# Kernel optimization log

Hardware: AMD Instinct MI355X
Metric: run time of the kernel (lower is better)

The kernel has to match this reference:

```python
import jax, jax.numpy as jnp
import numpy as np

CH_IN, CH_Y = 32, 16
B, H, W = 16, 256, 256


def setup_inputs() -> dict:
    key = jax.random.key(0)
    ks = jax.random.split(key, 10)
    scale_in = 1.0 / np.sqrt(CH_IN)
    scale_y = 1.0 / np.sqrt(CH_Y)
    return {
        "c": jax.random.normal(ks[0], (B, CH_IN, H, W), dtype=jnp.float32),
        "p": jax.random.normal(ks[1], (B, CH_IN, H, W), dtype=jnp.float32),
        "Wq": jax.random.uniform(ks[2], (CH_Y, CH_IN), jnp.float32, -scale_in, scale_in),
        "bq": jax.random.uniform(ks[3], (CH_Y,), jnp.float32, -scale_in, scale_in),
        "Wk": jax.random.uniform(ks[4], (CH_Y, CH_IN), jnp.float32, -scale_in, scale_in),
        "bk": jax.random.uniform(ks[5], (CH_Y,), jnp.float32, -scale_in, scale_in),
        "Wv": jax.random.uniform(ks[6], (CH_Y, CH_IN), jnp.float32, -scale_in, scale_in),
        "bv": jax.random.uniform(ks[7], (CH_Y,), jnp.float32, -scale_in, scale_in),
        "Wy": jax.random.uniform(ks[8], (CH_IN, CH_Y), jnp.float32, -scale_y, scale_y),
        "by": jax.random.uniform(ks[9], (CH_IN,), jnp.float32, -scale_y, scale_y),
    }


def _conv1x1(x, w, b):
    # x: [B,C,H,W], w: [O,C], b: [O] -> [B,O,H,W]
    return jnp.einsum("bchw,oc->bohw", x, w) + b[None, :, None, None]


def reference(c, p, Wq, bq, Wk, bk, Wv, bv, Wy, by):
    q = _conv1x1(c, Wq, bq)
    k = _conv1x1(p, Wk, bk)
    v = _conv1x1(p, Wv, bv)
    y = jax.nn.softmax(q * k, axis=-1)  # softmax over width
    y = y * v
    y = _conv1x1(y, Wy, by)
    return jnp.concatenate((y, c), axis=1)  # [B, 2*CH_IN, H, W]
```

## Files before the change

kernel.cpp:

```cpp
#include <hip/hip_runtime.h>

#define CH_IN 32
#define CH_Y  16
#define Bn    16
#define Hn    256
#define Wn    256
#define HW    (Hn * Wn)

typedef float f32x2 __attribute__((ext_vector_type(2)));

template<int ctrl, int rm, int bm>
__device__ __forceinline__ float dpp0(float x) {
    union { float f; int i; } u, r;
    u.f = x;
    r.i = __builtin_amdgcn_update_dpp(0, u.i, ctrl, rm, bm, false);
    return r.f;
}

__device__ __forceinline__ float wave_sum64(float x) {
    x += dpp0<0x111, 0xf, 0xf>(x);
    x += dpp0<0x112, 0xf, 0xf>(x);
    x += dpp0<0x114, 0xf, 0xf>(x);
    x += dpp0<0x118, 0xf, 0xf>(x);
    x += dpp0<0x142, 0xa, 0xf>(x);
    x += dpp0<0x143, 0xc, 0xf>(x);
    union { float f; int i; } u, r;
    u.f = x;
    r.i = __builtin_amdgcn_readlane(u.i, 63);
    return r.f;
}

__global__ __launch_bounds__(128, 4)
void CrossModalAttn_kernel(
    const float* __restrict__ cin, const float* __restrict__ pin,
    const float* __restrict__ Wq,  const float* __restrict__ bq,
    const float* __restrict__ Wk,  const float* __restrict__ bk,
    const float* __restrict__ Wv,  const float* __restrict__ bv,
    const float* __restrict__ Wy,  const float* __restrict__ by,
    float* __restrict__ out)
{
    const int bh   = blockIdx.x;
    const int b    = bh >> 8;
    const int h    = bh & 255;
    const int t    = threadIdx.x;
    const int wave = t >> 6;
    const int lane = t & 63;
    const int w0   = t << 1;

    const size_t rowoff = (size_t)h * Wn + w0;
    const float* pbase = pin + (size_t)b * CH_IN * HW + rowoff;
    const float* cbase = cin + (size_t)b * CH_IN * HW + rowoff;
    float*       obase = out + (size_t)b * (2 * CH_IN) * HW + rowoff;

    __shared__ float red[2 * CH_Y];

    f32x2 qe[CH_Y];
    #pragma unroll
    for (int o = 0; o < CH_Y; ++o) {
        float ti = bq[o];
        qe[o] = (f32x2){ti, ti};
    }
    #pragma unroll 8
    for (int cc = 0; cc < CH_IN; ++cc) {
        f32x2 x = *(const f32x2*)(cbase + (size_t)cc * HW);
        __builtin_nontemporal_store(
            x, (f32x2*)(obase + (size_t)(CH_IN + cc) * HW));
        #pragma unroll
        for (int o = 0; o < CH_Y; ++o) {
            float wgt = Wq[o * CH_IN + cc];
            qe[o].x = fmaf(wgt, x.x, qe[o].x);
            qe[o].y = fmaf(wgt, x.y, qe[o].y);
        }
    }

    f32x2 kk[CH_Y], vv[CH_Y];
    #pragma unroll
    for (int o = 0; o < CH_Y; ++o) {
        float tk = bk[o], tv = bv[o];
        kk[o] = (f32x2){tk, tk};
        vv[o] = (f32x2){tv, tv};
    }
    #pragma unroll 8
    for (int cc = 0; cc < CH_IN; ++cc) {
        f32x2 x = *(const f32x2*)(pbase + (size_t)cc * HW);
        #pragma unroll
        for (int o = 0; o < CH_Y; ++o) {
            float wk = Wk[o * CH_IN + cc];
            float wv = Wv[o * CH_IN + cc];
            kk[o].x = fmaf(wk, x.x, kk[o].x);
            kk[o].y = fmaf(wk, x.y, kk[o].y);
            vv[o].x = fmaf(wv, x.x, vv[o].x);
            vv[o].y = fmaf(wv, x.y, vv[o].y);
        }
    }

    #pragma unroll
    for (int o = 0; o < CH_Y; ++o) {
        f32x2 e;
        e.x = __expf(qe[o].x * kk[o].x);
        e.y = __expf(qe[o].y * kk[o].y);
        float ws = wave_sum64(e.x + e.y);
        if (lane == 0) red[wave * CH_Y + o] = ws;
        qe[o] = e;
    }
    __syncthreads();

    #pragma unroll
    for (int o = 0; o < CH_Y; ++o) {
        float tot = red[o] + red[CH_Y + o];
        float r = __builtin_amdgcn_rcpf(tot);
        qe[o].x *= r * vv[o].x;
        qe[o].y *= r * vv[o].y;
    }

    #pragma unroll 8
    for (int co = 0; co < CH_IN; ++co) {
        float ti = by[co];
        f32x2 acc = (f32x2){ti, ti};
        #pragma unroll
        for (int o = 0; o < CH_Y; ++o) {
            float wgt = Wy[co * CH_Y + o];
            acc.x = fmaf(wgt, qe[o].x, acc.x);
            acc.y = fmaf(wgt, qe[o].y, acc.y);
        }
        __builtin_nontemporal_store(
            acc, (f32x2*)(obase + (size_t)co * HW));
    }
}

extern "C" void kernel_launch(void* const* d_in, const int* in_sizes, int n_in,
                              void* d_out, int out_size, void* d_ws, size_t ws_size,
                              hipStream_t stream) {
    const float* c  = (const float*)d_in[0];
    const float* p  = (const float*)d_in[1];
    const float* Wq = (const float*)d_in[2];
    const float* bq = (const float*)d_in[3];
    const float* Wk = (const float*)d_in[4];
    const float* bk = (const float*)d_in[5];
    const float* Wv = (const float*)d_in[6];
    const float* bv = (const float*)d_in[7];
    const float* Wy = (const float*)d_in[8];
    const float* by = (const float*)d_in[9];
    float* out = (float*)d_out;

    dim3 grid(Bn * Hn);
    dim3 block(128);
    hipLaunchKernelGGL(CrossModalAttn_kernel, grid, block, 0, stream,
                       c, p, Wq, bq, Wk, bk, Wv, bv, Wy, by, out);
}
```

Baseline: 469.6 us.

## Split attention channels across waves with float4 per-lane row coverage

Each wave now covers the full 256-wide row (4 pixels per lane, float4 loads/stores) and takes half of the 16 attention channels, so each softmax sum needs only one intra-wave reduction and the cross-wave LDS combine goes away. The attention outputs are exchanged through a 16x256 LDS tile so that each wave then computes half of the 32 output channels. The trade is that both waves read the full c and p rows, doubling global load traffic (partly absorbed by cache), and the c passthrough store is split between the waves. Wider vector memory ops and fewer reduction steps are the intended gain.

```diff
diff --git a/kernel.cpp b/kernel.cpp
--- a/kernel.cpp
+++ b/kernel.cpp
@@ -7,7 +7,7 @@
 #define Wn    256
 #define HW    (Hn * Wn)
 
-typedef float f32x2 __attribute__((ext_vector_type(2)));
+typedef float f32x4 __attribute__((ext_vector_type(4)));
 
 template<int ctrl, int rm, int bm>
 __device__ __forceinline__ float dpp0(float x) {
@@ -43,88 +43,103 @@
     const int b    = bh >> 8;
     const int h    = bh & 255;
     const int t    = threadIdx.x;
-    const int wave = t >> 6;
     const int lane = t & 63;
-    const int w0   = t << 1;
+    const int wave = __builtin_amdgcn_readfirstlane(t >> 6);
+    const int w0   = lane << 2;
 
     const size_t rowoff = (size_t)h * Wn + w0;
     const float* pbase = pin + (size_t)b * CH_IN * HW + rowoff;
     const float* cbase = cin + (size_t)b * CH_IN * HW + rowoff;
     float*       obase = out + (size_t)b * (2 * CH_IN) * HW + rowoff;
 
-    __shared__ float red[2 * CH_Y];
+    __shared__ __align__(16) float yat_lds[CH_Y][Wn];
 
-    f32x2 qe[CH_Y];
+    const int o0 = wave << 3;
+
+    f32x4 qq[8];
     #pragma unroll
-    for (int o = 0; o < CH_Y; ++o) {
-        float ti = bq[o];
-        qe[o] = (f32x2){ti, ti};
+    for (int o = 0; o < 8; ++o) {
+        float ti = bq[o0 + o];
+        qq[o] = (f32x4){ti, ti, ti, ti};
     }
     #pragma unroll 8
     for (int cc = 0; cc < CH_IN; ++cc) {
-        f32x2 x = *(const f32x2*)(cbase + (size_t)cc * HW);
-        __builtin_nontemporal_store(
-            x, (f32x2*)(obase + (size_t)(CH_IN + cc) * HW));
+        f32x4 x = *(const f32x4*)(cbase + (size_t)cc * HW);
+        if ((cc >> 4) == wave)
+            __builtin_nontemporal_store(
+                x, (f32x4*)(obase + (size_t)(CH_IN + cc) * HW));
         #pragma unroll
-        for (int o = 0; o < CH_Y; ++o) {
-            float wgt = Wq[o * CH_IN + cc];
-            qe[o].x = fmaf(wgt, x.x, qe[o].x);
-            qe[o].y = fmaf(wgt, x.y, qe[o].y);
+        for (int o = 0; o < 8; ++o) {
+            float wgt = Wq[(o0 + o) * CH_IN + cc];
+            qq[o].x = fmaf(wgt, x.x, qq[o].x);
+            qq[o].y = fmaf(wgt, x.y, qq[o].y);
+            qq[o].z = fmaf(wgt, x.z, qq[o].z);
+            qq[o].w = fmaf(wgt, x.w, qq[o].w);
         }
     }
 
-    f32x2 kk[CH_Y], vv[CH_Y];
+    f32x4 kk[8], vv[8];
     #pragma unroll
-    for (int o = 0; o < CH_Y; ++o) {
-        float tk = bk[o], tv = bv[o];
-        kk[o] = (f32x2){tk, tk};
-        vv[o] = (f32x2){tv, tv};
+    for (int o = 0; o < 8; ++o) {
+        float tk = bk[o0 + o], tv = bv[o0 + o];
+        kk[o] = (f32x4){tk, tk, tk, tk};
+        vv[o] = (f32x4){tv, tv, tv, tv};
     }
     #pragma unroll 8
     for (int cc = 0; cc < CH_IN; ++cc) {
-        f32x2 x = *(const f32x2*)(pbase + (size_t)cc * HW);
+        f32x4 x = *(const f32x4*)(pbase + (size_t)cc * HW);
         #pragma unroll
-        for (int o = 0; o < CH_Y; ++o) {
-            float wk = Wk[o * CH_IN + cc];
-            float wv = Wv[o * CH_IN + cc];
+        for (int o = 0; o < 8; ++o) {
+            float wk = Wk[(o0 + o) * CH_IN + cc];
+            float wv = Wv[(o0 + o) * CH_IN + cc];
             kk[o].x = fmaf(wk, x.x, kk[o].x);
             kk[o].y = fmaf(wk, x.y, kk[o].y);
+            kk[o].z = fmaf(wk, x.z, kk[o].z);
+            kk[o].w = fmaf(wk, x.w, kk[o].w);
             vv[o].x = fmaf(wv, x.x, vv[o].x);
             vv[o].y = fmaf(wv, x.y, vv[o].y);
+            vv[o].z = fmaf(wv, x.z, vv[o].z);
+            vv[o].w = fmaf(wv, x.w, vv[o].w);
         }
     }
 
     #pragma unroll
-    for (int o = 0; o < CH_Y; ++o) {
-        f32x2 e;
-        e.x = __expf(qe[o].x * kk[o].x);
-        e.y = __expf(qe[o].y * kk[o].y);
-        float ws = wave_sum64(e.x + e.y);
-        if (lane == 0) red[wave * CH_Y + o] = ws;
-        qe[o] = e;
+    for (int o = 0; o < 8; ++o) {
+        f32x4 e;
+        e.x = __expf(qq[o].x * kk[o].x);
+        e.y = __expf(qq[o].y * kk[o].y);
+        e.z = __expf(qq[o].z * kk[o].z);
+        e.w = __expf(qq[o].w * kk[o].w);
+        float s = (e.x + e.y) + (e.z + e.w);
+        float r = __builtin_amdgcn_rcpf(wave_sum64(s));
+        e.x *= r * vv[o].x;
+        e.y *= r * vv[o].y;
+        e.z *= r * vv[o].z;
+        e.w *= r * vv[o].w;
+        *(f32x4*)&yat_lds[o0 + o][w0] = e;
     }
     __syncthreads();
 
+    f32x4 ya[CH_Y];
     #pragma unroll
-    for (int o = 0; o < CH_Y; ++o) {
-        float tot = red[o] + red[CH_Y + o];
-        float r = __builtin_amdgcn_rcpf(tot);
-        qe[o].x *= r * vv[o].x;
-        qe[o].y *= r * vv[o].y;
-    }
-
-    #pragma unroll 8
-    for (int co = 0; co < CH_IN; ++co) {
+    for (int o = 0; o < CH_Y; ++o)
+        ya[o] = *(const f32x4*)&yat_lds[o][w0];
+    const int co0 = wave << 4;
+    #pragma unroll 4
+    for (int ci = 0; ci < 16; ++ci) {
+        const int co = co0 + ci;
         float ti = by[co];
-        f32x2 acc = (f32x2){ti, ti};
+        f32x4 acc = (f32x4){ti, ti, ti, ti};
         #pragma unroll
         for (int o = 0; o < CH_Y; ++o) {
             float wgt = Wy[co * CH_Y + o];
-            acc.x = fmaf(wgt, qe[o].x, acc.x);
-            acc.y = fmaf(wgt, qe[o].y, acc.y);
+            acc.x = fmaf(wgt, ya[o].x, acc.x);
+            acc.y = fmaf(wgt, ya[o].y, acc.y);
+            acc.z = fmaf(wgt, ya[o].z, acc.z);
+            acc.w = fmaf(wgt, ya[o].w, acc.w);
         }
         __builtin_nontemporal_store(
-            acc, (f32x2*)(obase + (size_t)co * HW));
+            acc, (f32x4*)(obase + (size_t)co * HW));
     }
 }
 
```

New measurement: 508.0 us. 8.2% more time.
